# Kernel optimization log

Hardware: AMD Instinct MI355X
Metric: run time of the kernel (lower is better)

The kernel has to match this reference:

```python
import jax, jax.numpy as jnp
import numpy as np

B, NT, NC, NN = 2, 64, 1024, 1024
C, H = 1024, 16
HD = C // H
N = NT + NC + NN
EPS = 1e-5
NEG = -1e30


def _ln(t, w, b):
    # LayerNorm over last dim (head_dim), torch eps=1e-5
    mu = jnp.mean(t, axis=-1, keepdims=True)
    var = jnp.mean(jnp.square(t - mu), axis=-1, keepdims=True)
    return (t - mu) * jax.lax.rsqrt(var + EPS) * w + b


def _rope(q, k, pos):
    # q,k: [B,H,S,HD]; pos: [B,S]; rotate-half RoPE, base 10000
    hd = q.shape[-1]
    half = hd // 2
    inv_freq = 1.0 / (10000.0 ** (jnp.arange(half, dtype=jnp.float32) / half))
    ang = pos.astype(jnp.float32)[:, None, :, None] * inv_freq  # [B,1,S,half]
    cos, sin = jnp.cos(ang), jnp.sin(ang)
    def rot(t):
        t1, t2 = t[..., :half], t[..., half:]
        return jnp.concatenate([t1 * cos - t2 * sin, t2 * cos + t1 * sin], axis=-1)
    return rot(q), rot(k)


def setup_inputs() -> dict:
    key = jax.random.key(0)
    ks = jax.random.split(key, 4)
    s = 0.02
    return {
        "x": jax.random.normal(ks[0], (B, N, C), jnp.float32),
        "position_ids": jnp.broadcast_to(jnp.arange(NC + NN, dtype=jnp.int32), (B, NC + NN)),
        "text_position_ids": jnp.broadcast_to(jnp.arange(NT, dtype=jnp.int32), (B, NT)),
        "attention_mask": jnp.tril(jnp.ones((N, N), dtype=bool)),
        "n_text": NT, "n_clean": NC, "n_noised": NN,
        "qkv_w": jax.random.normal(ks[1], (3, 3 * C, C), jnp.float32) * s,
        "qkv_b": jnp.zeros((3, 3 * C), jnp.float32),
        "qn_w": jnp.ones((3, HD), jnp.float32),
        "qn_b": jnp.zeros((3, HD), jnp.float32),
        "kn_w": jnp.ones((3, HD), jnp.float32),
        "kn_b": jnp.zeros((3, HD), jnp.float32),
        "proj_w": jax.random.normal(ks[2], (3, C, C), jnp.float32) * s,
        "proj_b": jnp.zeros((3, C), jnp.float32),
    }


def reference(x, position_ids, text_position_ids, attention_mask, n_text, n_clean, n_noised,
              qkv_w, qkv_b, qn_w, qn_b, kn_w, kn_b, proj_w, proj_b):
    Bx, Nx, Cx = x.shape
    hd = qn_w.shape[-1]
    nh = Cx // hd
    b0, b1 = n_text, n_text + n_clean
    segs = (x[:, :b0], x[:, b0:b1], x[:, b1:])  # text / clean / noised

    qs, kks, vvs = [], [], []
    for i, xs in enumerate(segs):
        S = xs.shape[1]
        qkv = jnp.einsum('bsc,oc->bso', xs, qkv_w[i]) + qkv_b[i]
        qkv = qkv.reshape(Bx, S, 3, nh, hd).transpose(2, 0, 3, 1, 4)  # [3,B,H,S,hd]
        q = _ln(qkv[0], qn_w[i], qn_b[i])
        k = _ln(qkv[1], kn_w[i], kn_b[i])
        qs.append(q); kks.append(k); vvs.append(qkv[2])

    img_q = jnp.concatenate([qs[1], qs[2]], axis=2)
    img_k = jnp.concatenate([kks[1], kks[2]], axis=2)
    img_q, img_k = _rope(img_q, img_k, position_ids)
    txt_q, txt_k = _rope(qs[0], kks[0], text_position_ids)

    q = jnp.concatenate([txt_q, img_q], axis=2)
    k = jnp.concatenate([txt_k, img_k], axis=2)
    v = jnp.concatenate(vvs, axis=2)

    scale = 1.0 / np.sqrt(hd).astype(np.float32)
    scores = jnp.einsum('bhqd,bhkd->bhqk', q, k) * scale
    scores = jnp.where(attention_mask, scores, NEG)
    attn = jax.nn.softmax(scores, axis=-1)
    out = jnp.einsum('bhqk,bhkd->bhqd', attn, v)
    out = out.transpose(0, 2, 1, 3).reshape(Bx, Nx, Cx)

    o_segs = (out[:, :b0], out[:, b0:b1], out[:, b1:])
    outs = [jnp.einsum('bsc,oc->bso', o_segs[i], proj_w[i]) + proj_b[i] for i in range(3)]
    return jnp.concatenate(outs, axis=1)
```

## Files before the change

### kernel.cpp

```cpp
#include <hip/hip_runtime.h>
#include <hip/hip_bf16.h>

#define BB   2
#define NT   64
#define NC   1024
#define NN   1024
#define NTOK (NT + NC + NN)
#define CC   1024
#define HH   16
#define HD   64
#define K3   (3 * CC)
#define EPSV 1e-5f

typedef __attribute__((ext_vector_type(8))) short short8;
typedef __attribute__((ext_vector_type(4))) float f32x4;
typedef __attribute__((ext_vector_type(4))) float float4v;

__device__ __forceinline__ short bf16raw(float x) {
    __hip_bfloat16 h = __float2bfloat16(x);
    return *(short*)&h;
}

#define GL_LDS(gptr, lptr) \
    __builtin_amdgcn_global_load_lds( \
        (const __attribute__((address_space(1))) void*)(gptr), \
        (__attribute__((address_space(3))) void*)(lptr), 16, 0, 0)

#define WAIT_VM(N) asm volatile("s_waitcnt vmcnt(" #N ")" ::: "memory")
#define BARRIER_FENCED() do { __builtin_amdgcn_s_barrier(); \
                              asm volatile("" ::: "memory"); } while (0)
#define FENCE_BARRIER()  do { asm volatile("" ::: "memory"); \
                              __builtin_amdgcn_s_barrier(); } while (0)

__constant__ signed char QB_tab[33] =
    {16,16,16,15,15,15,14,14,14,13,13,13,12,12,12,11,11,10,10,9,9,8,8,7,7,6,6,5,4,3,2,1,0};
__constant__ signed char CH_tab[33] =
    { 0, 1, 2, 0, 1, 2, 0, 1, 2, 0, 1, 2, 0, 1, 2, 0, 1, 0, 1,0,1,0,1,0,1,0,1,0,0,0,0,0,0};

__global__ __launch_bounds__(256) void cast_all(
    const float* __restrict__ s0, const float* __restrict__ s1, const float* __restrict__ s2,
    __hip_bfloat16* __restrict__ d0, __hip_bfloat16* __restrict__ d1, __hip_bfloat16* __restrict__ d2,
    int n0, int n1, int n2)
{
    int i = blockIdx.x * 256 + threadIdx.x;
    int stride = gridDim.x * 256;
    int ntot = n0 + n1 + n2;
    for (; i < ntot; i += stride) {
        const float* sp; short* dp; int j;
        if (i < n0)            { sp = s0; dp = (short*)d0; j = i; }
        else if (i < n0 + n1)  { sp = s1; dp = (short*)d1; j = i - n0; }
        else                   { sp = s2; dp = (short*)d2; j = i - n0 - n1; }
        float4v v = *(const float4v*)(sp + (size_t)j * 4);
        short4 o;
        o.x = bf16raw(v.x); o.y = bf16raw(v.y); o.z = bf16raw(v.z); o.w = bf16raw(v.w);
        *(short4*)(dp + (size_t)j * 4) = o;
    }
}

__global__ __launch_bounds__(256) void gemm_qkv(
    const __hip_bfloat16* __restrict__ A,
    const __hip_bfloat16* __restrict__ Wb,
    const float* __restrict__ biasb,
    const float* __restrict__ qn_w, const float* __restrict__ qn_b,
    const float* __restrict__ kn_w, const float* __restrict__ kn_b,
    __hip_bfloat16* __restrict__ Q,
    __hip_bfloat16* __restrict__ Kg,
    __hip_bfloat16* __restrict__ Vt)
{
    __shared__ short lds[32768];
    short* buf = lds;

    int tid = threadIdx.x;
    int lane = tid & 63, w = tid >> 6;
    int l15 = lane & 15, quad = lane >> 4;
    int wm = w >> 1, wn = w & 1;
    int r7 = l15 & 7;

    int y = blockIdx.y;
    int seg, tm;
    if (y < 16)      { seg = 1; tm = y * 128; }
    else if (y < 32) { seg = 2; tm = (y - 16) * 128; }
    else             { seg = 0; tm = 0; }
    int S = (seg == 0) ? 64 : 1024;
    int seg_start = (seg == 0) ? 0 : (seg == 1 ? NT : NT + NC);
    const short* W = (const short*)Wb + (size_t)seg * K3 * CC;
    const float* bias = biasb + (size_t)seg * K3;
    int tileN = blockIdx.x * 128;

    const short* aptr[4];
    const short* bptr[4];
#pragma unroll
    for (int j = 0; j < 4; ++j) {
        int c = j * 256 + tid;
        int row = c >> 3, u = (c & 7) ^ (row & 7);
        int ar = tm + row;
        int arow = (ar / S) * NTOK + seg_start + (ar % S);
        aptr[j] = (const short*)A + (size_t)arow * CC + u * 8;
        bptr[j] = W + (size_t)(tileN + row) * CC + u * 8;
    }

    f32x4 zero = {0.f, 0.f, 0.f, 0.f};
    f32x4 acc[4][4];
#pragma unroll
    for (int mb = 0; mb < 4; ++mb)
#pragma unroll
        for (int nb = 0; nb < 4; ++nb) acc[mb][nb] = zero;

#pragma unroll
    for (int j = 0; j < 4; ++j) {
        int c8 = (j * 256 + tid) * 8;
        GL_LDS(aptr[j], lds + c8);
        GL_LDS(bptr[j], lds + 8192 + c8);
    }
    __syncthreads();

    for (int t = 0; t < 16; ++t) {
        short* As = lds + (t & 1) * 16384;
        short* Bs = As + 8192;
        if (t < 15) {
            short* An = lds + ((t + 1) & 1) * 16384;
            int k0 = (t + 1) * 64;
#pragma unroll
            for (int j = 0; j < 4; ++j) {
                int c8 = (j * 256 + tid) * 8;
                GL_LDS(aptr[j] + k0, An + c8);
                GL_LDS(bptr[j] + k0, An + 8192 + c8);
            }
            WAIT_VM(8);
        } else {
            WAIT_VM(0);
        }
        BARRIER_FENCED();

#pragma unroll
        for (int s = 0; s < 2; ++s) {
            int sx = ((s * 4 + quad) ^ r7) * 8;
            short8 af[4], bf[4];
#pragma unroll
            for (int mb = 0; mb < 4; ++mb)
                af[mb] = *(const short8*)&As[(wm * 64 + mb * 16 + l15) * 64 + sx];
#pragma unroll
            for (int nb = 0; nb < 4; ++nb)
                bf[nb] = *(const short8*)&Bs[(wn * 64 + nb * 16 + l15) * 64 + sx];
#pragma unroll
            for (int mb = 0; mb < 4; ++mb)
#pragma unroll
                for (int nb = 0; nb < 4; ++nb)
                    acc[mb][nb] = __builtin_amdgcn_mfma_f32_16x16x32_bf16(af[mb], bf[nb], acc[mb][nb], 0, 0, 0);
        }
        FENCE_BARRIER();
    }

    int sect = tileN >> 10;

    if (sect < 2) {
        const float* nw = (sect == 0 ? qn_w : kn_w) + seg * HD;
        const float* nbv = (sect == 0 ? qn_b : kn_b) + seg * HD;
        float lw[4], lb[4], bcol[4];
#pragma unroll
        for (int nb = 0; nb < 4; ++nb) {
            lw[nb] = nw[nb * 16 + l15];
            lb[nb] = nbv[nb * 16 + l15];
            bcol[nb] = bias[tileN + wn * 64 + nb * 16 + l15];
        }
        float qscale = (sect == 0) ? 0.18033688011112042f : 1.0f;

        float invf0 = expf(-9.210340371976184f * (float)l15 * (1.0f / 32.0f));
        float invf1 = expf(-9.210340371976184f * (float)(16 + l15) * (1.0f / 32.0f));
        float cd0, sd0, cd1, sd1;
        sincosf(invf0, &sd0, &cd0);
        sincosf(invf1, &sd1, &cd1);

#pragma unroll
        for (int mb = 0; mb < 4; ++mb) {
            int tok0 = wm * 64 + mb * 16 + quad * 4;
            int ar0 = tm + tok0;
            int nloc0 = ar0 % S;
            int pos0 = (seg == 0) ? nloc0 : (seg_start + nloc0 - NT);
            float c0, s0, c1, s1v;
            sincosf((float)pos0 * invf0, &s0, &c0);
            sincosf((float)pos0 * invf1, &s1v, &c1);

#pragma unroll
            for (int r = 0; r < 4; ++r) {
                int tok = tok0 + r;
                float v[4];
#pragma unroll
                for (int nb = 0; nb < 4; ++nb) v[nb] = acc[mb][nb][r] + bcol[nb];

                float t1 = v[0] + v[1] + v[2] + v[3];
                float t2 = v[0] * v[0] + v[1] * v[1] + v[2] * v[2] + v[3] * v[3];
#pragma unroll
                for (int off = 8; off >= 1; off >>= 1) {
                    t1 += __shfl_xor(t1, off);
                    t2 += __shfl_xor(t2, off);
                }
                float mu = t1 * (1.0f / 64.0f);
                float var = t2 * (1.0f / 64.0f) - mu * mu;
                float rstd = rsqrtf(var + EPSV);
#pragma unroll
                for (int nb = 0; nb < 4; ++nb) v[nb] = (v[nb] - mu) * rstd * lw[nb] + lb[nb];

                short* bp = &buf[tok * 134 + wn * 64];
                bp[0 * 16 + l15] = bf16raw((v[0] * c0 - v[2] * s0) * qscale);
                bp[1 * 16 + l15] = bf16raw((v[1] * c1 - v[3] * s1v) * qscale);
                bp[2 * 16 + l15] = bf16raw((v[2] * c0 + v[0] * s0) * qscale);
                bp[3 * 16 + l15] = bf16raw((v[3] * c1 + v[1] * s1v) * qscale);

                float nc0 = c0 * cd0 - s0 * sd0, ns0 = s0 * cd0 + c0 * sd0;
                float nc1 = c1 * cd1 - s1v * sd1, ns1 = s1v * cd1 + c1 * sd1;
                c0 = nc0; s0 = ns0; c1 = nc1; s1v = ns1;
            }
        }
        __syncthreads();
        __hip_bfloat16* dst = (sect == 0) ? Q : Kg;
        int head_base = (tileN & 1023) >> 6;
#pragma unroll
        for (int it = 0; it < 8; ++it) {
            int idx = it * 256 + tid;
            int tok = idx >> 4, cc = (idx & 15) * 8;
            int ar = tm + tok;
            int bb = ar / S;
            int nloc = seg_start + (ar % S);
            int hh2 = head_base + (cc >> 6), d = cc & 63;
            *(short8*)((short*)dst + ((size_t)(bb * HH + hh2) * NTOK + nloc) * HD + d) =
                *(const short8*)&buf[tok * 134 + cc];
        }
    } else {
        float bcol[4];
#pragma unroll
        for (int nb = 0; nb < 4; ++nb) bcol[nb] = bias[tileN + wn * 64 + nb * 16 + l15];
#pragma unroll
        for (int mb = 0; mb < 4; ++mb) {
#pragma unroll
            for (int r = 0; r < 4; ++r) {
                int tok = wm * 64 + mb * 16 + quad * 4 + r;
#pragma unroll
                for (int nb = 0; nb < 4; ++nb) {
                    int col = wn * 64 + nb * 16 + l15;
                    buf[col * 134 + tok] = bf16raw(acc[mb][nb][r] + bcol[nb]);
                }
            }
        }
        __syncthreads();
#pragma unroll
        for (int it = 0; it < 8; ++it) {
            int idx = it * 256 + tid;
            int row = idx >> 4;
            int tc = (idx & 15) * 8;
            int vcol = (tileN - 2048) + row;
            int h = vcol >> 6, d = vcol & 63;
            int ar = tm + tc;
            int bb = ar / S;
            int nloc = seg_start + (ar % S);
            short8 val = *(const short8*)&buf[row * 134 + tc];
            *(short8*)((short*)Vt + ((size_t)(bb * HH + h) * HD + d) * NTOK + nloc) = val;
        }
    }
}

__global__ __launch_bounds__(256) void gemm_proj(
    const __hip_bfloat16* __restrict__ A,
    const __hip_bfloat16* __restrict__ Wb,
    const float* __restrict__ biasb,
    float* __restrict__ Cout)
{
    __shared__ short lds[24576];

    int tid = threadIdx.x;
    int lane = tid & 63, w = tid >> 6;
    int l15 = lane & 15, quad = lane >> 4;
    int wm = w >> 1, wn = w & 1;
    int r7 = l15 & 7;

    int y = blockIdx.y;
    int seg, tm;
    if (y < 32)      { seg = 1; tm = y * 64; }
    else if (y < 64) { seg = 2; tm = (y - 32) * 64; }
    else             { seg = 0; tm = (y - 64) * 64; }
    int S = (seg == 0) ? 64 : 1024;
    int seg_start = (seg == 0) ? 0 : (seg == 1 ? NT : NT + NC);
    const short* W = (const short*)Wb + (size_t)seg * CC * CC;
    const float* bias = biasb + (size_t)seg * CC;
    int tileN = blockIdx.x * 128;

    const short* aptr[2];
    const short* bptr[4];
#pragma unroll
    for (int j = 0; j < 2; ++j) {
        int c = j * 256 + tid;
        int row = c >> 3, u = (c & 7) ^ (row & 7);
        int ar = tm + row;
        int arow = (ar / S) * NTOK + seg_start + (ar % S);
        aptr[j] = (const short*)A + (size_t)arow * CC + u * 8;
    }
#pragma unroll
    for (int j = 0; j < 4; ++j) {
        int c = j * 256 + tid;
        int row = c >> 3, u = (c & 7) ^ (row & 7);
        bptr[j] = W + (size_t)(tileN + row) * CC + u * 8;
    }

    f32x4 zero = {0.f, 0.f, 0.f, 0.f};
    f32x4 acc[2][4];
#pragma unroll
    for (int mb = 0; mb < 2; ++mb)
#pragma unroll
        for (int nb = 0; nb < 4; ++nb) acc[mb][nb] = zero;

#pragma unroll
    for (int j = 0; j < 2; ++j)
        GL_LDS(aptr[j], lds + (j * 256 + tid) * 8);
#pragma unroll
    for (int j = 0; j < 4; ++j)
        GL_LDS(bptr[j], lds + 4096 + (j * 256 + tid) * 8);
    __syncthreads();

    for (int t = 0; t < 16; ++t) {
        short* As = lds + (t & 1) * 12288;
        short* Bs = As + 4096;
        if (t < 15) {
            short* An = lds + ((t + 1) & 1) * 12288;
            int k0 = (t + 1) * 64;
#pragma unroll
            for (int j = 0; j < 2; ++j)
                GL_LDS(aptr[j] + k0, An + (j * 256 + tid) * 8);
#pragma unroll
            for (int j = 0; j < 4; ++j)
                GL_LDS(bptr[j] + k0, An + 4096 + (j * 256 + tid) * 8);
            WAIT_VM(6);
        } else {
            WAIT_VM(0);
        }
        BARRIER_FENCED();

#pragma unroll
        for (int s = 0; s < 2; ++s) {
            int sx = ((s * 4 + quad) ^ r7) * 8;
            short8 af[2], bf[4];
#pragma unroll
            for (int mb = 0; mb < 2; ++mb)
                af[mb] = *(const short8*)&As[(wm * 32 + mb * 16 + l15) * 64 + sx];
#pragma unroll
            for (int nb = 0; nb < 4; ++nb)
                bf[nb] = *(const short8*)&Bs[(wn * 64 + nb * 16 + l15) * 64 + sx];
#pragma unroll
            for (int mb = 0; mb < 2; ++mb)
#pragma unroll
                for (int nb = 0; nb < 4; ++nb)
                    acc[mb][nb] = __builtin_amdgcn_mfma_f32_16x16x32_bf16(af[mb], bf[nb], acc[mb][nb], 0, 0, 0);
        }
        FENCE_BARRIER();
    }

#pragma unroll
    for (int mb = 0; mb < 2; ++mb) {
#pragma unroll
        for (int r = 0; r < 4; ++r) {
            int ar = tm + wm * 32 + mb * 16 + quad * 4 + r;
            int crow = (ar / S) * NTOK + seg_start + (ar % S);
            float* cp = Cout + (size_t)crow * CC + tileN;
#pragma unroll
            for (int nb = 0; nb < 4; ++nb) {
                int col = wn * 64 + nb * 16 + l15;
                cp[col] = acc[mb][nb][r] + bias[tileN + col];
            }
        }
    }
}

__global__ __launch_bounds__(512) void attn_part(
    const __hip_bfloat16* __restrict__ Q,
    const __hip_bfloat16* __restrict__ Kg,
    const __hip_bfloat16* __restrict__ Vt,
    __hip_bfloat16* __restrict__ O,
    float* __restrict__ Opart,
    float* __restrict__ lpart)
{
    __shared__ short Ks[2][4096];
    __shared__ short Vs[2][4096];
    __shared__ short Ps[8][16 * 72];

    int tid = threadIdx.x;
    int lane = tid & 63, w = tid >> 6;
    int quad = lane >> 4, l15 = lane & 15;
    int r7 = l15 & 7;
    int bh = blockIdx.y, b = bh >> 4, h = bh & 15;

    int e = blockIdx.x;
    int qb = QB_tab[e], c = CH_tab[e];
    int q0 = qb * 128;
    int nt = 2 * qb + 2; if (nt > 33) nt = 33;
    int t0 = c * 12, t1 = t0 + 12; if (t1 > nt) t1 = nt;
    bool direct = (nt <= 12);

    size_t base = (size_t)bh * NTOK * HD;

    int qrow = q0 + w * 16 + l15;
    int qr_c = qrow < NTOK ? qrow : NTOK - 1;
    short8 qf0 = *(const short8*)((const short*)Q + base + (size_t)qr_c * HD + quad * 8);
    short8 qf1 = *(const short8*)((const short*)Q + base + (size_t)qr_c * HD + 32 + quad * 8);

    int srow = tid >> 3;
    int su = (tid & 7) ^ (srow & 7);
    const short* kptr = (const short*)Kg + base + (size_t)srow * HD + su * 8;
    const short* vptr = (const short*)Vt + base + (size_t)srow * NTOK + su * 8;
    int c8 = tid * 8;

    f32x4 zero = {0.f, 0.f, 0.f, 0.f};
    f32x4 oacc[4] = {zero, zero, zero, zero};
    float l[4] = {0.f, 0.f, 0.f, 0.f};

    int qmin_w = q0 + w * 16;
    int qmax_w = qmin_w + 15;
    int sx0 = (quad ^ r7) * 8;
    int sx1 = ((4 + quad) ^ r7) * 8;

    GL_LDS(kptr + (size_t)(t0 * 64) * HD, Ks[0] + c8);
    GL_LDS(vptr + t0 * 64, Vs[0] + c8);
    __syncthreads();

    int cur = 0;
    for (int t = t0; t < t1; ++t) {
        if (t + 1 < t1) {
            GL_LDS(kptr + (size_t)((t + 1) * 64) * HD, Ks[cur ^ 1] + c8);
            GL_LDS(vptr + (t + 1) * 64, Vs[cur ^ 1] + c8);
            WAIT_VM(2);
        } else {
            WAIT_VM(0);
        }
        BARRIER_FENCED();

        if (t * 64 <= qmax_w) {
            f32x4 s[4];
            __builtin_amdgcn_s_setprio(1);
#pragma unroll
            for (int kb = 0; kb < 4; ++kb) {
                int krow = (kb * 16 + l15) * 64;
                short8 kf0 = *(const short8*)&Ks[cur][krow + sx0];
                short8 kf1 = *(const short8*)&Ks[cur][krow + sx1];
                f32x4 z = zero;
                z = __builtin_amdgcn_mfma_f32_16x16x32_bf16(qf0, kf0, z, 0, 0, 0);
                z = __builtin_amdgcn_mfma_f32_16x16x32_bf16(qf1, kf1, z, 0, 0, 0);
                s[kb] = z;
            }
            __builtin_amdgcn_s_setprio(0);

            if (t * 64 + 63 <= qmin_w) {
#pragma unroll
                for (int r = 0; r < 4; ++r)
#pragma unroll
                    for (int kb = 0; kb < 4; ++kb) {
                        float p = __builtin_amdgcn_exp2f(s[kb][r]);
                        Ps[w][(quad * 4 + r) * 72 + kb * 16 + l15] = bf16raw(p);
                        l[r] += p;
                    }
            } else {
#pragma unroll
                for (int r = 0; r < 4; ++r) {
                    int qg = q0 + w * 16 + quad * 4 + r;
#pragma unroll
                    for (int kb = 0; kb < 4; ++kb) {
                        int kgk = t * 64 + kb * 16 + l15;
                        float p = (kgk <= qg) ? __builtin_amdgcn_exp2f(s[kb][r]) : 0.f;
                        Ps[w][(quad * 4 + r) * 72 + kb * 16 + l15] = bf16raw(p);
                        l[r] += p;
                    }
                }
            }

            __builtin_amdgcn_wave_barrier();

            __builtin_amdgcn_s_setprio(1);
#pragma unroll
            for (int sl = 0; sl < 2; ++sl) {
                short8 pf = *(const short8*)&Ps[w][l15 * 72 + sl * 32 + quad * 8];
                int vsx = ((sl * 4 + quad) ^ r7) * 8;
#pragma unroll
                for (int db = 0; db < 4; ++db) {
                    short8 vf = *(const short8*)&Vs[cur][(db * 16 + l15) * 64 + vsx];
                    oacc[db] = __builtin_amdgcn_mfma_f32_16x16x32_bf16(pf, vf, oacc[db], 0, 0, 0);
                }
            }
            __builtin_amdgcn_s_setprio(0);
        }

        FENCE_BARRIER();
        cur ^= 1;
    }

#pragma unroll
    for (int r = 0; r < 4; ++r) {
#pragma unroll
        for (int off = 8; off >= 1; off >>= 1) l[r] += __shfl_xor(l[r], off);
    }

    if (direct) {
#pragma unroll
        for (int r = 0; r < 4; ++r) {
            int qg = q0 + w * 16 + quad * 4 + r;
            float inv_l = 1.0f / l[r];
#pragma unroll
            for (int db = 0; db < 4; ++db) {
                O[(size_t)(b * NTOK + qg) * CC + h * HD + db * 16 + l15] =
                    __float2bfloat16(oacc[db][r] * inv_l);
            }
        }
    } else {
        int pidx = (bh * 17 + qb) * 3 + c;
        float* op = Opart + (size_t)pidx * (128 * 64);
#pragma unroll
        for (int r = 0; r < 4; ++r) {
            int q = w * 16 + quad * 4 + r;
#pragma unroll
            for (int db = 0; db < 4; ++db)
                op[q * 64 + db * 16 + l15] = oacc[db][r];
            if (l15 == 0) lpart[pidx * 128 + q] = l[r];
        }
    }
}

__global__ __launch_bounds__(512) void attn_comb(
    const float* __restrict__ Opart, const float* __restrict__ lpart,
    __hip_bfloat16* __restrict__ O)
{
    __shared__ float ls[128];
    int tid = threadIdx.x;
    int qb = 6 + blockIdx.x;
    int bh = blockIdx.y, b = bh >> 4, h = bh & 15;
    int nt = 2 * qb + 2; if (nt > 33) nt = 33;
    int nch = (nt + 11) / 12;
    int q0 = qb * 128;
    int pbase = (bh * 17 + qb) * 3;

    if (tid < 128) {
        float s = 0.f;
        for (int cc = 0; cc < nch; ++cc) s += lpart[(pbase + cc) * 128 + tid];
        ls[tid] = 1.0f / s;
    }
    __syncthreads();

#pragma unroll
    for (int k = 0; k < 16; ++k) {
        int elem = k * 512 + tid;
        int q = elem >> 6, d = elem & 63;
        int qg = q0 + q;
        if (qg >= NTOK) continue;
        float s = 0.f;
        for (int cc = 0; cc < nch; ++cc)
            s += Opart[(size_t)(pbase + cc) * (128 * 64) + elem];
        O[(size_t)(b * NTOK + qg) * CC + h * HD + d] = __float2bfloat16(s * ls[q]);
    }
}

extern "C" void kernel_launch(void* const* d_in, const int* in_sizes, int n_in,
                              void* d_out, int out_size, void* d_ws, size_t ws_size,
                              hipStream_t stream) {
    const float* x      = (const float*)d_in[0];
    const float* qkv_w  = (const float*)d_in[7];
    const float* qkv_b  = (const float*)d_in[8];
    const float* qn_w   = (const float*)d_in[9];
    const float* qn_b   = (const float*)d_in[10];
    const float* kn_w   = (const float*)d_in[11];
    const float* kn_b   = (const float*)d_in[12];
    const float* proj_w = (const float*)d_in[13];
    const float* proj_b = (const float*)d_in[14];
    float* out = (float*)d_out;

    const size_t n_x    = (size_t)BB * NTOK * CC;
    const size_t n_qkvw = (size_t)3 * K3 * CC;
    const size_t n_prjw = (size_t)3 * CC * CC;
    const size_t n_part = (size_t)32 * 17 * 3;

    __hip_bfloat16* x_bf    = (__hip_bfloat16*)d_ws;
    __hip_bfloat16* qkvw_bf = x_bf + n_x;
    __hip_bfloat16* prjw_bf = qkvw_bf + n_qkvw;
    __hip_bfloat16* Qbf  = prjw_bf + n_prjw;
    __hip_bfloat16* Kbf  = Qbf + n_x;
    __hip_bfloat16* Vtbf = Kbf + n_x;
    float* Opart = (float*)(Vtbf + n_x);
    float* lpart = Opart + n_part * (128 * 64);
    __hip_bfloat16* attn_bf = x_bf;

    cast_all<<<1024, 256, 0, stream>>>(x, qkv_w, proj_w, x_bf, qkvw_bf, prjw_bf,
                                       (int)(n_x / 4), (int)(n_qkvw / 4), (int)(n_prjw / 4));

    gemm_qkv<<<dim3(K3 / 128, 33), 256, 0, stream>>>(
        x_bf, qkvw_bf, qkv_b,
        qn_w, qn_b, kn_w, kn_b, Qbf, Kbf, Vtbf);

    attn_part<<<dim3(33, BB * HH), 512, 0, stream>>>(Qbf, Kbf, Vtbf, attn_bf, Opart, lpart);

    attn_comb<<<dim3(11, BB * HH), 512, 0, stream>>>(Opart, lpart, attn_bf);

    gemm_proj<<<dim3(CC / 128, 66), 256, 0, stream>>>(attn_bf, prjw_bf, proj_b, out);
}
```

Measured before the change: 270.4 us.

## Fuse attention split-combine into projection GEMM A-tile staging

Drops the separate attn_comb kernel. For query blocks whose attention was split into partial chunks, gemm_proj now sums the fp32 partial outputs and normalisers, normalises, converts to bf16 and writes the A tile into LDS itself instead of loading it from global memory. This removes one launch and the round trip of the combined bf16 tensor through global memory. In exchange, each of the 8 N-tile blocks repeats the combine for its rows, the partial reads are synchronous register loads instead of async LDS loads, and the explicit vmcnt waits plus fenced barriers in both the GEMM and attention loops are replaced by plain __syncthreads.

After: 275.2 us. Within noise of the previous version (+1.8%).

```diff
diff --git a/kernel.cpp b/kernel.cpp
--- a/kernel.cpp
+++ b/kernel.cpp
@@ -263,6 +263,8 @@
     const __hip_bfloat16* __restrict__ A,
     const __hip_bfloat16* __restrict__ Wb,
     const float* __restrict__ biasb,
+    const float* __restrict__ Opart,
+    const float* __restrict__ lpart,
     float* __restrict__ Cout)
 {
     __shared__ short lds[24576];
@@ -284,16 +286,25 @@
     const float* bias = biasb + (size_t)seg * CC;
     int tileN = blockIdx.x * 128;
 
+    int b_blk = tm / S;
+    int tok0 = seg_start + (tm % S);
+    int qb_blk = tok0 >> 7;
+    int nt = 2 * qb_blk + 2; if (nt > 33) nt = 33;
+    int nch = (nt + 11) / 12;
+    bool direct = (nt <= 12);
+
     const short* aptr[2];
-    const short* bptr[4];
+    int rowj[2], uj[2];
 #pragma unroll
     for (int j = 0; j < 2; ++j) {
         int c = j * 256 + tid;
         int row = c >> 3, u = (c & 7) ^ (row & 7);
+        rowj[j] = row; uj[j] = u;
         int ar = tm + row;
         int arow = (ar / S) * NTOK + seg_start + (ar % S);
         aptr[j] = (const short*)A + (size_t)arow * CC + u * 8;
     }
+    const short* bptr[4];
 #pragma unroll
     for (int j = 0; j < 4; ++j) {
         int c = j * 256 + tid;
@@ -301,6 +312,31 @@
         bptr[j] = W + (size_t)(tileN + row) * CC + u * 8;
     }
 
+    auto stage_comb = [&](int h, short* dst) {
+        int pb = ((b_blk * HH + h) * 17 + qb_blk) * 3;
+#pragma unroll
+        for (int j = 0; j < 2; ++j) {
+            int trow = (tok0 & 127) + rowj[j];
+            float ls = 0.f;
+            float4v v0 = {0.f, 0.f, 0.f, 0.f}, v1 = {0.f, 0.f, 0.f, 0.f};
+            for (int cc = 0; cc < nch; ++cc) {
+                ls += lpart[(size_t)(pb + cc) * 128 + trow];
+                const float* op = Opart + (size_t)(pb + cc) * 8192 + trow * 64 + uj[j] * 8;
+                float4v a0 = *(const float4v*)op;
+                float4v a1 = *(const float4v*)(op + 4);
+                v0.x += a0.x; v0.y += a0.y; v0.z += a0.z; v0.w += a0.w;
+                v1.x += a1.x; v1.y += a1.y; v1.z += a1.z; v1.w += a1.w;
+            }
+            float inv = 1.0f / ls;
+            short8 o;
+            o[0] = bf16raw(v0.x * inv); o[1] = bf16raw(v0.y * inv);
+            o[2] = bf16raw(v0.z * inv); o[3] = bf16raw(v0.w * inv);
+            o[4] = bf16raw(v1.x * inv); o[5] = bf16raw(v1.y * inv);
+            o[6] = bf16raw(v1.z * inv); o[7] = bf16raw(v1.w * inv);
+            *(short8*)(dst + (j * 256 + tid) * 8) = o;
+        }
+    };
+
     f32x4 zero = {0.f, 0.f, 0.f, 0.f};
     f32x4 acc[2][4];
 #pragma unroll
@@ -308,9 +344,13 @@
 #pragma unroll
         for (int nb = 0; nb < 4; ++nb) acc[mb][nb] = zero;
 
-#pragma unroll
-    for (int j = 0; j < 2; ++j)
-        GL_LDS(aptr[j], lds + (j * 256 + tid) * 8);
+    if (direct) {
+#pragma unroll
+        for (int j = 0; j < 2; ++j)
+            GL_LDS(aptr[j], lds + (j * 256 + tid) * 8);
+    } else {
+        stage_comb(0, lds);
+    }
 #pragma unroll
     for (int j = 0; j < 4; ++j)
         GL_LDS(bptr[j], lds + 4096 + (j * 256 + tid) * 8);
@@ -319,20 +359,20 @@
     for (int t = 0; t < 16; ++t) {
         short* As = lds + (t & 1) * 12288;
         short* Bs = As + 4096;
+        short* An = lds + ((t + 1) & 1) * 12288;
         if (t < 15) {
-            short* An = lds + ((t + 1) & 1) * 12288;
             int k0 = (t + 1) * 64;
-#pragma unroll
-            for (int j = 0; j < 2; ++j)
-                GL_LDS(aptr[j] + k0, An + (j * 256 + tid) * 8);
+            if (direct) {
+#pragma unroll
+                for (int j = 0; j < 2; ++j)
+                    GL_LDS(aptr[j] + k0, An + (j * 256 + tid) * 8);
+            } else {
+                stage_comb(t + 1, An);
+            }
 #pragma unroll
             for (int j = 0; j < 4; ++j)
                 GL_LDS(bptr[j] + k0, An + 4096 + (j * 256 + tid) * 8);
-            WAIT_VM(6);
-        } else {
-            WAIT_VM(0);
-        }
-        BARRIER_FENCED();
+        }
 
 #pragma unroll
         for (int s = 0; s < 2; ++s) {
@@ -350,7 +390,7 @@
                 for (int nb = 0; nb < 4; ++nb)
                     acc[mb][nb] = __builtin_amdgcn_mfma_f32_16x16x32_bf16(af[mb], bf[nb], acc[mb][nb], 0, 0, 0);
         }
-        FENCE_BARRIER();
+        __syncthreads();
     }
 
 #pragma unroll
@@ -425,11 +465,7 @@
         if (t + 1 < t1) {
             GL_LDS(kptr + (size_t)((t + 1) * 64) * HD, Ks[cur ^ 1] + c8);
             GL_LDS(vptr + (t + 1) * 64, Vs[cur ^ 1] + c8);
-            WAIT_VM(2);
-        } else {
-            WAIT_VM(0);
-        }
-        BARRIER_FENCED();
+        }
 
         if (t * 64 <= qmax_w) {
             f32x4 s[4];
@@ -485,7 +521,7 @@
             __builtin_amdgcn_s_setprio(0);
         }
 
-        FENCE_BARRIER();
+        __syncthreads();
         cur ^= 1;
     }
 
@@ -517,39 +553,6 @@
                 op[q * 64 + db * 16 + l15] = oacc[db][r];
             if (l15 == 0) lpart[pidx * 128 + q] = l[r];
         }
-    }
-}
-
-__global__ __launch_bounds__(512) void attn_comb(
-    const float* __restrict__ Opart, const float* __restrict__ lpart,
-    __hip_bfloat16* __restrict__ O)
-{
-    __shared__ float ls[128];
-    int tid = threadIdx.x;
-    int qb = 6 + blockIdx.x;
-    int bh = blockIdx.y, b = bh >> 4, h = bh & 15;
-    int nt = 2 * qb + 2; if (nt > 33) nt = 33;
-    int nch = (nt + 11) / 12;
-    int q0 = qb * 128;
-    int pbase = (bh * 17 + qb) * 3;
-
-    if (tid < 128) {
-        float s = 0.f;
-        for (int cc = 0; cc < nch; ++cc) s += lpart[(pbase + cc) * 128 + tid];
-        ls[tid] = 1.0f / s;
-    }
-    __syncthreads();
-
-#pragma unroll
-    for (int k = 0; k < 16; ++k) {
-        int elem = k * 512 + tid;
-        int q = elem >> 6, d = elem & 63;
-        int qg = q0 + q;
-        if (qg >= NTOK) continue;
-        float s = 0.f;
-        for (int cc = 0; cc < nch; ++cc)
-            s += Opart[(size_t)(pbase + cc) * (128 * 64) + elem];
-        O[(size_t)(b * NTOK + qg) * CC + h * HD + d] = __float2bfloat16(s * ls[q]);
     }
 }
 
@@ -591,7 +594,6 @@
 
     attn_part<<<dim3(33, BB * HH), 512, 0, stream>>>(Qbf, Kbf, Vtbf, attn_bf, Opart, lpart);
 
-    attn_comb<<<dim3(11, BB * HH), 512, 0, stream>>>(Opart, lpart, attn_bf);
-
-    gemm_proj<<<dim3(CC / 128, 66), 256, 0, stream>>>(attn_bf, prjw_bf, proj_b, out);
+    gemm_proj<<<dim3(CC / 128, 66), 256, 0, stream>>>(attn_bf, prjw_bf, proj_b,
+                                                      Opart, lpart, out);
 }
```
